# Kernel optimization log

Measured on AMD Instinct MI355X. Metric: run time of the kernel, lower is better.

The kernel has to match this reference:

```python
import jax, jax.numpy as jnp
import numpy as np

FP8_E4M3_MAX = 448.0  # torch.float8_e4m3fn max


def _fp8_quant(x, scale):
    # per-tensor static-scale fp8 quantization: clamp(x/scale) -> e4m3 -> back to f32
    q = jnp.clip(x / scale, -FP8_E4M3_MAX, FP8_E4M3_MAX)
    return q.astype(jnp.float8_e4m3fn).astype(jnp.float32)


def setup_inputs() -> dict:
    key = jax.random.key(0)
    k1, k2, k3 = jax.random.split(key, 3)
    M, K, N = 8192, 4096, 11008
    inp = jax.random.normal(k1, (M, K), dtype=jnp.float32)
    # weight is stored pre-quantized (fp8 values held as fp32), already transposed to [K, N]
    w = jax.random.normal(k2, (K, N), dtype=jnp.float32) * 0.02
    weight_scale = jnp.float32(0.01)
    qweight = _fp8_quant(w, weight_scale)
    qbias = jax.random.normal(k3, (N,), dtype=jnp.float32) * 0.01
    input_scale = jnp.float32(0.05)
    return {
        "input": inp,
        "qweight": qweight,
        "qbias": qbias,
        "weight_scale": weight_scale,
        "input_scale": input_scale,
    }


def reference(input, qweight, qbias, weight_scale, input_scale) -> jnp.ndarray:
    # scaled_fp8_quant with a provided static scale: x_scale == input_scale
    qinput = _fp8_quant(input, input_scale)  # [M, K], fp8 values in f32
    # cutlass_scaled_mm / _scaled_mm: (qinput * x_scale) @ (qweight * weight_scale) + bias
    out = jnp.einsum("mk,kn->mn", qinput, qweight) * (input_scale * weight_scale)
    out = out + qbias[None, :]
    return out.astype(input.dtype)
```

## Files before the change

kernel.cpp:

```cpp
#include <hip/hip_runtime.h>

typedef float v16f __attribute__((ext_vector_type(16)));
typedef int   v8i  __attribute__((ext_vector_type(8)));
typedef int   v4i  __attribute__((ext_vector_type(4)));

#define BM 256
#define BN 256
#define SC1 0x7F7F7FFu + 0x7F000000u

static constexpr unsigned SCONE = 0x7F7F7F7Fu;

__device__ __forceinline__ unsigned int pack4_fp8(float a, float b, float c, float d) {
    unsigned int v = __builtin_amdgcn_cvt_pk_fp8_f32(a, b, 0, false);
    v = __builtin_amdgcn_cvt_pk_fp8_f32(c, d, v, true);
    return v;
}

__global__ __launch_bounds__(256) void quant_x_kernel(
    const float* __restrict__ X, const float* __restrict__ sp,
    unsigned int* __restrict__ Q)
{
    const long i = (long)blockIdx.x * 256 + threadIdx.x;
    const float s = sp[0];
    const float4 v = ((const float4*)X)[i];
    const float a = fminf(fmaxf(v.x / s, -448.f), 448.f);
    const float b = fminf(fmaxf(v.y / s, -448.f), 448.f);
    const float c = fminf(fmaxf(v.z / s, -448.f), 448.f);
    const float d = fminf(fmaxf(v.w / s, -448.f), 448.f);
    Q[i] = pack4_fp8(a, b, c, d);
}

__global__ __launch_bounds__(256) void quant_wT_kernel(
    const float* __restrict__ Wf, unsigned char* __restrict__ Wq, int K, int N)
{
    __shared__ float T[64][68];
    const int tid = threadIdx.x;
    const int k0 = blockIdx.x * 64;
    const int n0 = blockIdx.y * 64;
    const int rr = tid >> 4;
    const int cc = (tid & 15) * 4;
#pragma unroll
    for (int j = 0; j < 4; ++j) {
        const int r = j * 16 + rr;
        const float4 v = *(const float4*)(Wf + (long)(k0 + r) * N + n0 + cc);
        T[r][cc + 0] = v.x; T[r][cc + 1] = v.y; T[r][cc + 2] = v.z; T[r][cc + 3] = v.w;
    }
    __syncthreads();
    const int n  = tid >> 2;
    const int kc = (tid & 3) * 16;
    unsigned int o[4];
#pragma unroll
    for (int q = 0; q < 4; ++q)
        o[q] = pack4_fp8(T[kc + q*4 + 0][n], T[kc + q*4 + 1][n],
                         T[kc + q*4 + 2][n], T[kc + q*4 + 3][n]);
    uint4 out; out.x = o[0]; out.y = o[1]; out.z = o[2]; out.w = o[3];
    *(uint4*)(Wq + (long)(n0 + n) * K + k0 + kc) = out;
}

__device__ __forceinline__ void async_copy16(const void* g, void* l) {
    __builtin_amdgcn_global_load_lds(
        (const __attribute__((address_space(1))) unsigned int*)g,
        (__attribute__((address_space(3))) unsigned int*)l,
        16, 0, 0);
}

__device__ __forceinline__ v8i ld32(const unsigned char* p, int o0, int o1) {
    const v4i lo = *(const v4i*)(p + o0);
    const v4i hi = *(const v4i*)(p + o1);
    v8i f; f[0]=lo[0]; f[1]=lo[1]; f[2]=lo[2]; f[3]=lo[3];
           f[4]=hi[0]; f[5]=hi[1]; f[6]=hi[2]; f[7]=hi[3];
    return f;
}

__global__ __launch_bounds__(512, 2) void fp8_gemm_kernel(
    const unsigned char* __restrict__ A8,
    const unsigned char* __restrict__ B8,
    const float* __restrict__ bias,
    const float* __restrict__ ws_p, const float* __restrict__ is_p,
    float* __restrict__ C, int M, int N, int K)
{
    __shared__ unsigned char AsB[2 * 32768];
    __shared__ unsigned char BsB[2 * 32768];

    const int tid = threadIdx.x;
    const int l   = tid & 63;
    const int w   = tid >> 6;
    const int wr  = w >> 2, wc = w & 3;
    const int lrow = l & 31;
    const int h    = l >> 5;
    const int sw   = lrow & 7;

    int bx = blockIdx.x, by = blockIdx.y;
    {
        const int gx = gridDim.x, nwg = gridDim.x * gridDim.y;
        if ((nwg & 7) == 0) {
            const int id  = by * gx + bx;
            const int cpx = nwg >> 3;
            const int swz = (id & 7) * cpx + (id >> 3);
            bx = swz % gx;
            by = swz / gx;
        }
    }
    const long m0 = (long)by * BM;
    const long n0 = (long)bx * BN;

    const int  chOff = (((tid & 7) ^ ((tid >> 3) & 7)) << 4);
    const long K64  = (long)64  * K;
    const long K32  = (long)32  * K;
    const long K128 = (long)128 * K;
    const unsigned char* aSrc = A8 + (m0 + (tid >> 3)) * (long)K + chOff;
    const unsigned char* bSrc = B8 + (n0 + (tid >> 8) * 64 + ((tid >> 3) & 31)) * (long)K + chOff;
    const int bDst = (tid >> 8) * 8192 + ((tid >> 3) & 31) * 128 + (tid & 7) * 16;

    unsigned char* As0 = AsB;          unsigned char* As1 = AsB + 32768;
    unsigned char* Bs0 = BsB;          unsigned char* Bs1 = BsB + 32768;

    const int aRdBase = (wr * 128 + lrow) * 128;
    const int bRdBase = (wc * 64  + lrow) * 128;
    const int c00 = (((0 + h*2 + 0) ^ sw) << 4);
    const int c01 = (((0 + h*2 + 1) ^ sw) << 4);
    const int c10 = (((4 + h*2 + 0) ^ sw) << 4);
    const int c11 = (((4 + h*2 + 1) ^ sw) << 4);

    v16f acc[4][2];
#pragma unroll
    for (int i = 0; i < 4; ++i)
#pragma unroll
        for (int j = 0; j < 2; ++j)
#pragma unroll
            for (int e = 0; e < 16; ++e)
                acc[i][j][e] = 0.f;

#define STAGE_A(DSTBASE, QM, TBYTE) do { \
    const unsigned char* s_ = aSrc + (TBYTE) + (QM) * K64; \
    async_copy16(s_,        (DSTBASE) + (QM) * 8192 + tid * 16); \
    async_copy16(s_ + K128, (DSTBASE) + 16384 + (QM) * 8192 + tid * 16); \
} while (0)

#define STAGE_B(DSTBASE, QN, TBYTE) do { \
    const unsigned char* s_ = bSrc + (TBYTE) + (QN) * K32; \
    async_copy16(s_,        (DSTBASE) + (QN) * 4096 + bDst); \
    async_copy16(s_ + K128, (DSTBASE) + 16384 + (QN) * 4096 + bDst); \
} while (0)

#define MFMA(AV, BV, D) \
    D = __builtin_amdgcn_mfma_scale_f32_32x32x64_f8f6f4( \
        (AV), (BV), (D), 0, 0, 0, SCONE, 0, SCONE)

#define PHASE(ABUF, BBUF, QM, QN, STAGE_CODE, WAIT_CODE) do { \
    const unsigned char* Ab_ = (ABUF); \
    const unsigned char* Bb_ = (BBUF); \
    const v8i a0k0 = ld32(Ab_ + aRdBase + (QM)*8192,        c00, c01); \
    const v8i a0k1 = ld32(Ab_ + aRdBase + (QM)*8192,        c10, c11); \
    const v8i a1k0 = ld32(Ab_ + aRdBase + (QM)*8192 + 4096, c00, c01); \
    const v8i a1k1 = ld32(Ab_ + aRdBase + (QM)*8192 + 4096, c10, c11); \
    const v8i b0   = ld32(Bb_ + bRdBase + (QN)*4096,        c00, c01); \
    const v8i b1   = ld32(Bb_ + bRdBase + (QN)*4096,        c10, c11); \
    STAGE_CODE; \
    __builtin_amdgcn_s_barrier(); \
    asm volatile("s_waitcnt lgkmcnt(0)" ::: "memory"); \
    __builtin_amdgcn_sched_barrier(0); \
    __builtin_amdgcn_s_setprio(1); \
    MFMA(a0k0, b0, acc[(QM)*2 + 0][QN]); \
    MFMA(a1k0, b0, acc[(QM)*2 + 1][QN]); \
    MFMA(a0k1, b1, acc[(QM)*2 + 0][QN]); \
    MFMA(a1k1, b1, acc[(QM)*2 + 1][QN]); \
    __builtin_amdgcn_s_setprio(0); \
    __builtin_amdgcn_sched_barrier(0); \
    WAIT_CODE; \
    __builtin_amdgcn_s_barrier(); \
    __builtin_amdgcn_sched_barrier(0); \
} while (0)

    STAGE_A(As0, 0, 0);   STAGE_B(Bs0, 0, 0);
    STAGE_A(As0, 1, 0);   STAGE_B(Bs0, 1, 0);
    STAGE_A(As1, 0, 128); STAGE_B(Bs1, 0, 128);
    asm volatile("s_waitcnt vmcnt(4)" ::: "memory");
    __builtin_amdgcn_s_barrier();

    const int NIT = K >> 8;
    for (int it = 0; it < NIT; ++it) {
        const long tB = (long)it << 8;
        const bool lst = (it == NIT - 1);

        PHASE(As0, Bs0, 0, 0, { STAGE_A(As1, 1, tB + 128); }, {});
        PHASE(As0, Bs0, 0, 1, { STAGE_B(Bs1, 1, tB + 128); }, {});
        PHASE(As0, Bs0, 1, 0, { if (!lst) STAGE_A(As0, 0, tB + 256); }, {});
        PHASE(As0, Bs0, 1, 1, { if (!lst) STAGE_B(Bs0, 0, tB + 256); },
              { if (!lst) { asm volatile("s_waitcnt vmcnt(4)" ::: "memory"); }
                else      { asm volatile("s_waitcnt vmcnt(0)" ::: "memory"); } });
        PHASE(As1, Bs1, 0, 0, { if (!lst) STAGE_A(As0, 1, tB + 256); }, {});
        PHASE(As1, Bs1, 0, 1, { if (!lst) STAGE_B(Bs0, 1, tB + 256); }, {});
        PHASE(As1, Bs1, 1, 0, { if (!lst) STAGE_A(As1, 0, tB + 384); }, {});
        PHASE(As1, Bs1, 1, 1, { if (!lst) STAGE_B(Bs1, 0, tB + 384); },
              { if (!lst) { asm volatile("s_waitcnt vmcnt(4)" ::: "memory"); } });
    }

#undef PHASE
#undef MFMA
#undef STAGE_A
#undef STAGE_B

    const float s = is_p[0] * ws_p[0];
#pragma unroll
    for (int mt = 0; mt < 4; ++mt)
#pragma unroll
        for (int nt = 0; nt < 2; ++nt) {
            const long cc = n0 + wc * 64 + nt * 32 + lrow;
            const float bv = bias[cc];
            float* dst = C + (m0 + wr * 128 + mt * 32 + h * 4) * (long)N + cc;
#pragma unroll
            for (int g = 0; g < 4; ++g)
#pragma unroll
                for (int r = 0; r < 4; ++r)
                    dst[(long)(g * 8 + r) * N] = acc[mt][nt][g * 4 + r] * s + bv;
        }
}

extern "C" void kernel_launch(void* const* d_in, const int* in_sizes, int n_in,
                              void* d_out, int out_size, void* d_ws, size_t ws_size,
                              hipStream_t stream)
{
    const float* X    = (const float*)d_in[0];
    const float* Wf   = (const float*)d_in[1];
    const float* bias = (const float*)d_in[2];
    const float* wsc  = (const float*)d_in[3];
    const float* isc  = (const float*)d_in[4];
    float* out = (float*)d_out;

    const int N = in_sizes[2];
    const int K = in_sizes[1] / N;
    const int M = in_sizes[0] / K;

    unsigned char* A8 = (unsigned char*)d_ws;
    unsigned char* B8 = A8 + (size_t)M * K;

    quant_x_kernel<<<dim3((unsigned)((long)M * K / 4 / 256)), 256, 0, stream>>>(
        X, isc, (unsigned int*)A8);

    quant_wT_kernel<<<dim3(K / 64, N / 64), 256, 0, stream>>>(Wf, B8, K, N);

    fp8_gemm_kernel<<<dim3(N / BN, M / BM), 512, 0, stream>>>(
        A8, B8, bias, wsc, isc, out, M, N, K);
}
```

Before: 1.173 ms.

## Use 4-wave blocks with 128x128 per-wave tiles and simple double-buffered K loop

The GEMM block shrinks from 8 waves to 4 waves, so each wave now computes a 128x128 output tile (4x4 MFMA tiles) instead of 128x64. The eight-phase interleaved pipeline with per-phase barriers and priority hints is replaced by a plain double-buffered loop: stage the whole next K=128 tile, wait, barrier, then run 32 MFMAs. The intent is more register-level reuse of A/B fragments and fewer barriers per MFMA. In exchange, occupancy drops (launch bounds 256,1 and large accumulators), and the fine-grained interleaving of loads with compute is lost.

```diff
diff --git a/kernel.cpp b/kernel.cpp
--- a/kernel.cpp
+++ b/kernel.cpp
@@ -6,7 +6,8 @@
 
 #define BM 256
 #define BN 256
-#define SC1 0x7F7F7FFu + 0x7F000000u
+#define BKB 128
+#define TILE_BYTES 32768
 
 static constexpr unsigned SCONE = 0x7F7F7F7Fu;
 
@@ -72,20 +73,20 @@
     return f;
 }
 
-__global__ __launch_bounds__(512, 2) void fp8_gemm_kernel(
+__global__ __launch_bounds__(256, 1) void fp8_gemm_kernel(
     const unsigned char* __restrict__ A8,
     const unsigned char* __restrict__ B8,
     const float* __restrict__ bias,
     const float* __restrict__ ws_p, const float* __restrict__ is_p,
     float* __restrict__ C, int M, int N, int K)
 {
-    __shared__ unsigned char AsB[2 * 32768];
-    __shared__ unsigned char BsB[2 * 32768];
+    __shared__ unsigned char AsB[2 * TILE_BYTES];
+    __shared__ unsigned char BsB[2 * TILE_BYTES];
 
     const int tid = threadIdx.x;
     const int l   = tid & 63;
     const int w   = tid >> 6;
-    const int wr  = w >> 2, wc = w & 3;
+    const int wr  = w >> 1, wc = w & 1;
     const int lrow = l & 31;
     const int h    = l >> 5;
     const int sw   = lrow & 7;
@@ -105,108 +106,98 @@
     const long n0 = (long)bx * BN;
 
     const int  chOff = (((tid & 7) ^ ((tid >> 3) & 7)) << 4);
-    const long K64  = (long)64  * K;
-    const long K32  = (long)32  * K;
-    const long K128 = (long)128 * K;
+    const long rowStep = (long)32 * K;
     const unsigned char* aSrc = A8 + (m0 + (tid >> 3)) * (long)K + chOff;
-    const unsigned char* bSrc = B8 + (n0 + (tid >> 8) * 64 + ((tid >> 3) & 31)) * (long)K + chOff;
-    const int bDst = (tid >> 8) * 8192 + ((tid >> 3) & 31) * 128 + (tid & 7) * 16;
-
-    unsigned char* As0 = AsB;          unsigned char* As1 = AsB + 32768;
-    unsigned char* Bs0 = BsB;          unsigned char* Bs1 = BsB + 32768;
-
-    const int aRdBase = (wr * 128 + lrow) * 128;
-    const int bRdBase = (wc * 64  + lrow) * 128;
-    const int c00 = (((0 + h*2 + 0) ^ sw) << 4);
-    const int c01 = (((0 + h*2 + 1) ^ sw) << 4);
-    const int c10 = (((4 + h*2 + 0) ^ sw) << 4);
-    const int c11 = (((4 + h*2 + 1) ^ sw) << 4);
-
-    v16f acc[4][2];
+    const unsigned char* bSrc = B8 + (n0 + (tid >> 3)) * (long)K + chOff;
+
+    const int c0s = (((0 + 2*h + 0) ^ sw) << 4);
+    const int c1s = (((0 + 2*h + 1) ^ sw) << 4);
+    const int c2s = (((4 + 2*h + 0) ^ sw) << 4);
+    const int c3s = (((4 + 2*h + 1) ^ sw) << 4);
+
+    int offA[4], offB[4];
+#pragma unroll
+    for (int mt = 0; mt < 4; ++mt) offA[mt] = (wr * 128 + mt * 32 + lrow) * BKB;
+#pragma unroll
+    for (int nt = 0; nt < 4; ++nt) offB[nt] = (wc * 128 + nt * 32 + lrow) * BKB;
+
+    v16f acc[4][4];
 #pragma unroll
     for (int i = 0; i < 4; ++i)
 #pragma unroll
-        for (int j = 0; j < 2; ++j)
+        for (int j = 0; j < 4; ++j)
 #pragma unroll
             for (int e = 0; e < 16; ++e)
                 acc[i][j][e] = 0.f;
-
-#define STAGE_A(DSTBASE, QM, TBYTE) do { \
-    const unsigned char* s_ = aSrc + (TBYTE) + (QM) * K64; \
-    async_copy16(s_,        (DSTBASE) + (QM) * 8192 + tid * 16); \
-    async_copy16(s_ + K128, (DSTBASE) + 16384 + (QM) * 8192 + tid * 16); \
-} while (0)
-
-#define STAGE_B(DSTBASE, QN, TBYTE) do { \
-    const unsigned char* s_ = bSrc + (TBYTE) + (QN) * K32; \
-    async_copy16(s_,        (DSTBASE) + (QN) * 4096 + bDst); \
-    async_copy16(s_ + K128, (DSTBASE) + 16384 + (QN) * 4096 + bDst); \
-} while (0)
 
 #define MFMA(AV, BV, D) \
     D = __builtin_amdgcn_mfma_scale_f32_32x32x64_f8f6f4( \
         (AV), (BV), (D), 0, 0, 0, SCONE, 0, SCONE)
 
-#define PHASE(ABUF, BBUF, QM, QN, STAGE_CODE, WAIT_CODE) do { \
-    const unsigned char* Ab_ = (ABUF); \
-    const unsigned char* Bb_ = (BBUF); \
-    const v8i a0k0 = ld32(Ab_ + aRdBase + (QM)*8192,        c00, c01); \
-    const v8i a0k1 = ld32(Ab_ + aRdBase + (QM)*8192,        c10, c11); \
-    const v8i a1k0 = ld32(Ab_ + aRdBase + (QM)*8192 + 4096, c00, c01); \
-    const v8i a1k1 = ld32(Ab_ + aRdBase + (QM)*8192 + 4096, c10, c11); \
-    const v8i b0   = ld32(Bb_ + bRdBase + (QN)*4096,        c00, c01); \
-    const v8i b1   = ld32(Bb_ + bRdBase + (QN)*4096,        c10, c11); \
-    STAGE_CODE; \
-    __builtin_amdgcn_s_barrier(); \
-    asm volatile("s_waitcnt lgkmcnt(0)" ::: "memory"); \
-    __builtin_amdgcn_sched_barrier(0); \
-    __builtin_amdgcn_s_setprio(1); \
-    MFMA(a0k0, b0, acc[(QM)*2 + 0][QN]); \
-    MFMA(a1k0, b0, acc[(QM)*2 + 1][QN]); \
-    MFMA(a0k1, b1, acc[(QM)*2 + 0][QN]); \
-    MFMA(a1k1, b1, acc[(QM)*2 + 1][QN]); \
-    __builtin_amdgcn_s_setprio(0); \
-    __builtin_amdgcn_sched_barrier(0); \
-    WAIT_CODE; \
-    __builtin_amdgcn_s_barrier(); \
-    __builtin_amdgcn_sched_barrier(0); \
-} while (0)
-
-    STAGE_A(As0, 0, 0);   STAGE_B(Bs0, 0, 0);
-    STAGE_A(As0, 1, 0);   STAGE_B(Bs0, 1, 0);
-    STAGE_A(As1, 0, 128); STAGE_B(Bs1, 0, 128);
-    asm volatile("s_waitcnt vmcnt(4)" ::: "memory");
-    __builtin_amdgcn_s_barrier();
-
-    const int NIT = K >> 8;
-    for (int it = 0; it < NIT; ++it) {
-        const long tB = (long)it << 8;
-        const bool lst = (it == NIT - 1);
-
-        PHASE(As0, Bs0, 0, 0, { STAGE_A(As1, 1, tB + 128); }, {});
-        PHASE(As0, Bs0, 0, 1, { STAGE_B(Bs1, 1, tB + 128); }, {});
-        PHASE(As0, Bs0, 1, 0, { if (!lst) STAGE_A(As0, 0, tB + 256); }, {});
-        PHASE(As0, Bs0, 1, 1, { if (!lst) STAGE_B(Bs0, 0, tB + 256); },
-              { if (!lst) { asm volatile("s_waitcnt vmcnt(4)" ::: "memory"); }
-                else      { asm volatile("s_waitcnt vmcnt(0)" ::: "memory"); } });
-        PHASE(As1, Bs1, 0, 0, { if (!lst) STAGE_A(As0, 1, tB + 256); }, {});
-        PHASE(As1, Bs1, 0, 1, { if (!lst) STAGE_B(Bs0, 1, tB + 256); }, {});
-        PHASE(As1, Bs1, 1, 0, { if (!lst) STAGE_A(As1, 0, tB + 384); }, {});
-        PHASE(As1, Bs1, 1, 1, { if (!lst) STAGE_B(Bs1, 0, tB + 384); },
-              { if (!lst) { asm volatile("s_waitcnt vmcnt(4)" ::: "memory"); } });
+    auto stage = [&](long ktB, int slot) {
+        unsigned char* al = AsB + slot * TILE_BYTES + tid * 16;
+        unsigned char* bl = BsB + slot * TILE_BYTES + tid * 16;
+        const unsigned char* ag = aSrc + ktB;
+        const unsigned char* bg = bSrc + ktB;
+#pragma unroll
+        for (int j = 0; j < 8; ++j)
+            async_copy16(ag + j * rowStep, al + j * 4096);
+#pragma unroll
+        for (int j = 0; j < 8; ++j)
+            async_copy16(bg + j * rowStep, bl + j * 4096);
+    };
+
+    const int NT = K / BKB;
+    stage(0, 0);
+
+    for (int t = 0; t < NT; ++t) {
+        if (t + 1 < NT) {
+            stage((long)(t + 1) * BKB, (t + 1) & 1);
+            asm volatile("s_waitcnt vmcnt(16)" ::: "memory");
+        } else {
+            asm volatile("s_waitcnt vmcnt(0)" ::: "memory");
+        }
+        __builtin_amdgcn_s_barrier();
+
+        const unsigned char* Ab = AsB + (t & 1) * TILE_BYTES;
+        const unsigned char* Bb = BsB + (t & 1) * TILE_BYTES;
+
+        {
+            v8i a[4], b[4];
+#pragma unroll
+            for (int mt = 0; mt < 4; ++mt) a[mt] = ld32(Ab + offA[mt], c0s, c1s);
+#pragma unroll
+            for (int nt = 0; nt < 4; ++nt) b[nt] = ld32(Bb + offB[nt], c0s, c1s);
+#pragma unroll
+            for (int mt = 0; mt < 4; ++mt)
+#pragma unroll
+                for (int nt = 0; nt < 4; ++nt)
+                    MFMA(a[mt], b[nt], acc[mt][nt]);
+        }
+        {
+            v8i a[4], b[4];
+#pragma unroll
+            for (int mt = 0; mt < 4; ++mt) a[mt] = ld32(Ab + offA[mt], c2s, c3s);
+#pragma unroll
+            for (int nt = 0; nt < 4; ++nt) b[nt] = ld32(Bb + offB[nt], c2s, c3s);
+#pragma unroll
+            for (int mt = 0; mt < 4; ++mt)
+#pragma unroll
+                for (int nt = 0; nt < 4; ++nt)
+                    MFMA(a[mt], b[nt], acc[mt][nt]);
+        }
+
+        __builtin_amdgcn_sched_barrier(0);
+        __builtin_amdgcn_s_barrier();
     }
-
-#undef PHASE
 #undef MFMA
-#undef STAGE_A
-#undef STAGE_B
 
     const float s = is_p[0] * ws_p[0];
 #pragma unroll
     for (int mt = 0; mt < 4; ++mt)
 #pragma unroll
-        for (int nt = 0; nt < 2; ++nt) {
-            const long cc = n0 + wc * 64 + nt * 32 + lrow;
+        for (int nt = 0; nt < 4; ++nt) {
+            const long cc = n0 + wc * 128 + nt * 32 + lrow;
             const float bv = bias[cc];
             float* dst = C + (m0 + wr * 128 + mt * 32 + h * 4) * (long)N + cc;
 #pragma unroll
@@ -240,6 +231,6 @@
 
     quant_wT_kernel<<<dim3(K / 64, N / 64), 256, 0, stream>>>(Wf, B8, K, N);
 
-    fp8_gemm_kernel<<<dim3(N / BN, M / BM), 512, 0, stream>>>(
+    fp8_gemm_kernel<<<dim3(N / BN, M / BM), 256, 0, stream>>>(
         A8, B8, bias, wsc, isc, out, M, N, K);
 }
```

New measurement: 1.010 ms. -14.0%, faster.
